# Performance work log

Measured on AMD Instinct MI355X. Metric: run time of the kernel, lower is better.

Reference implementation:

```python
import jax, jax.numpy as jnp
import numpy as np

B, C, H, W = 8, 192, 128, 128
NH, WS, PS = 6, 8, 8
HD = C // NH
SCALE = HD ** -0.5

def _rel_pos_log(ws):
    # log-spaced signed relative coordinates, [N, N, 2]
    coords = np.stack(np.meshgrid(np.arange(ws), np.arange(ws), indexing='ij'))
    cf = coords.reshape(2, -1)
    rp = (cf[:, :, None] - cf[:, None, :]).transpose(1, 2, 0).astype(np.float32)
    return jnp.asarray(np.sign(rp) * np.log1p(np.abs(rp)))

def setup_inputs() -> dict:
    key = jax.random.key(0)
    ks = jax.random.split(key, 8)
    s = 0.02
    return {
        'x': jax.random.normal(ks[0], (B, C, H, W), jnp.float32),
        'V_w': jax.random.normal(ks[1], (C, C), jnp.float32) * s,
        'V_b': jnp.zeros((C,), jnp.float32),
        'QK_w': jax.random.normal(ks[2], (2 * C, C), jnp.float32) * s,
        'QK_b': jnp.zeros((2 * C,), jnp.float32),
        'proj_w': jax.random.normal(ks[3], (C, C), jnp.float32) * s,
        'proj_b': jnp.zeros((C,), jnp.float32),
        'meta_w1': jax.random.normal(ks[4], (2, 256), jnp.float32) * s,
        'meta_b1': jnp.zeros((256,), jnp.float32),
        'meta_w2': jax.random.normal(ks[5], (256, NH), jnp.float32) * s,
        'meta_b2': jnp.zeros((NH,), jnp.float32),
    }

def reference(x, V_w, V_b, QK_w, QK_b, proj_w, proj_b, meta_w1, meta_b1, meta_w2, meta_b2):
    N = WS * WS
    # 1x1 convs for V and QK
    v = jnp.einsum('bchw,oc->bohw', x, V_w) + V_b[None, :, None, None]
    qk = jnp.einsum('bchw,oc->bohw', x, QK_w) + QK_b[None, :, None, None]
    qkv = jnp.concatenate([qk, v], axis=1)  # [B, 3C, H, W]
    # window partition -> [B * nW, N, 3C]
    t = qkv.transpose(0, 2, 3, 1).reshape(B, H // WS, WS, W // WS, WS, 3 * C)
    wins = t.transpose(0, 1, 3, 2, 4, 5).reshape(-1, N, 3 * C)
    B_ = wins.shape[0]
    qkv3 = wins.reshape(B_, N, 3, NH, HD).transpose(2, 0, 3, 1, 4)
    q, k, vv = qkv3[0] * SCALE, qkv3[1], qkv3[2]  # [B_, NH, N, HD]
    # FFT cross-modulation of q and k over the 8x8 window grid (c = N/64 = 1)
    cg = N // (PS * PS)
    qp = q.reshape(B_, NH, cg, PS, PS, HD).transpose(0, 1, 2, 5, 3, 4)
    kp = k.reshape(B_, NH, cg, PS, PS, HD).transpose(0, 1, 2, 5, 3, 4)
    o = jnp.fft.irfft2(jnp.fft.rfft2(qp) * jnp.fft.rfft2(kp), s=(PS, PS))
    o = o.transpose(0, 1, 2, 4, 5, 3).reshape(B_, NH, N, HD)
    # relative position bias from meta MLP on log-spaced coords
    rp = _rel_pos_log(WS)  # [N, N, 2]
    bias = jax.nn.relu(rp @ meta_w1 + meta_b1) @ meta_w2 + meta_b2  # [N, N, NH]
    bias = bias.transpose(2, 0, 1)  # [NH, N, N]
    attn = jnp.einsum('bhnd,bhmd->bhnm', o, vv) + bias[None]
    attn = jax.nn.softmax(attn, axis=-1)
    y = jnp.einsum('bhnm,bhmd->bhnd', attn, vv).transpose(0, 2, 1, 3).reshape(B_, N, C)
    # window reverse -> [B, C, H, W]
    y = y.reshape(B, H // WS, W // WS, WS, WS, C).transpose(0, 1, 3, 2, 4, 5).reshape(B, H, W, C)
    y = y.transpose(0, 3, 1, 2)
    return jnp.einsum('bchw,oc->bohw', y, proj_w) + proj_b[None, :, None, None]
```

## Files before the change

### kernel.cpp

```cpp
#include <hip/hip_runtime.h>

#define SCALEQ 0.17677669529663687f

typedef __bf16 bf16x8 __attribute__((ext_vector_type(8)));
typedef __bf16 bf16x2 __attribute__((ext_vector_type(2)));
typedef float f32x4 __attribute__((ext_vector_type(4)));
typedef float f32x2 __attribute__((ext_vector_type(2)));

__device__ __forceinline__ float bflo(unsigned int u) { return __uint_as_float(u << 16); }
__device__ __forceinline__ float bfhi(unsigned int u) { return __uint_as_float(u & 0xffff0000u); }
__device__ __forceinline__ f32x2 b2x2(unsigned int u) {
    f32x2 r; r[0] = bflo(u); r[1] = bfhi(u); return r;
}
__device__ __forceinline__ unsigned short f2b(float f) {
    return __builtin_bit_cast(unsigned short, (__bf16)f);
}
__device__ __forceinline__ unsigned int pk2(float a, float b) {
    bf16x2 v; v[0] = (__bf16)a; v[1] = (__bf16)b;
    return __builtin_bit_cast(unsigned int, v);
}

#define RA     0
#define RB     24576
#define RC     49152
#define LDS_BYTES 73728

#define WS_WQKV_ELEMS 110592
#define WS_WP_OFF_EL  110592
#define WS_B2_OFF_B   294912
#define WS_YB_OFF_B   393216
#define WS_TOTAL_B    50724864

__device__ __forceinline__ bf16x8 ldsf(const char* p) {
    uint4 u = *(const uint4*)p;
    return __builtin_bit_cast(bf16x8, u);
}
__device__ __forceinline__ bf16x8 gldf(const unsigned short* p) {
    uint4 u = *(const uint4*)p;
    return __builtin_bit_cast(bf16x8, u);
}

__global__ void wprep_kernel(const float* __restrict__ QKw, const float* __restrict__ Vw,
                             const float* __restrict__ Pw, unsigned short* __restrict__ wsb) {
    int i = blockIdx.x * 256 + threadIdx.x;
    if (i >= 147456) return;
    if (i < WS_WQKV_ELEMS) {
        int r = i / 192, c = i - r * 192;
        float v = (r < 384) ? QKw[r * 192 + c] : Vw[(r - 384) * 192 + c];
        if (r < 192) v *= SCALEQ;
        wsb[i] = f2b(v);
    } else {
        int j = i - WS_WQKV_ELEMS;
        wsb[WS_WP_OFF_EL + j] = f2b(Pw[j]);
    }
}

__global__ void bias2_kernel(const float* __restrict__ Mw1, const float* __restrict__ Mb1,
                             const float* __restrict__ Mw2, const float* __restrict__ Mb2,
                             float* __restrict__ out) {
    int i = blockIdx.x * 256 + threadIdx.x;
    if (i >= 6 * 64 * 64) return;
    int h = i >> 12, n = (i >> 6) & 63, m = i & 63;
    float dy = (float)((n >> 3) - (m >> 3));
    float dx = (float)((n & 7) - (m & 7));
    float f0 = copysignf(log1pf(fabsf(dy)), dy);
    float f1 = copysignf(log1pf(fabsf(dx)), dx);
    float a = Mb2[h];
    for (int u = 0; u < 256; ++u) {
        float hv = fmaxf(f0 * Mw1[u] + f1 * Mw1[256 + u] + Mb1[u], 0.0f);
        a = fmaf(hv, Mw2[u * 6 + h], a);
    }
    out[i] = a;
}

__global__ __launch_bounds__(512, 4)
void fused_win_attn(const float* __restrict__ x,
                    const float* __restrict__ Vb, const float* __restrict__ QKb,
                    const float* __restrict__ Pb,
                    const unsigned short* __restrict__ wqkv,
                    const unsigned short* __restrict__ wp,
                    const float* __restrict__ bias2,
                    char* __restrict__ yb,
                    float* __restrict__ out,
                    int split)
{
    extern __shared__ char smem[];
    const int t   = threadIdx.x;
    const int wv  = t >> 6;
    const int l15 = t & 15;
    const int l4  = (t >> 4) & 3;

    const int wid = ((blockIdx.x & 7) << 8) | (blockIdx.x >> 3);
    const int b   = wid >> 8;
    const int wy  = (wid >> 4) & 15;
    const int wx  = wid & 15;
    const int y0  = wy * 8, x0 = wx * 8;

    const f32x4 zz = {0.0f, 0.0f, 0.0f, 0.0f};

    {
        const float* xb = x + (size_t)b * 192 * 16384;
        #pragma unroll
        for (int i = 0; i < 6; ++i) {
            int idx = t + 512 * i;
            int c = idx >> 4, sub = idx & 15;
            int r = sub >> 1, hf = sub & 1;
            float4 v4 = *(const float4*)(xb + c * 16384 + (y0 + r) * 128 + x0 + hf * 4);
            int n0 = r * 8 + hf * 4;
            unsigned short sv[4] = {f2b(v4.x), f2b(v4.y), f2b(v4.z), f2b(v4.w)};
            #pragma unroll
            for (int e = 0; e < 4; ++e) {
                int n = n0 + e;
                *(unsigned short*)(smem + RA + ((n * 384 + c * 2) ^ ((n & 7) << 4))) = sv[e];
            }
        }
    }
    __syncthreads();

    const int wcol = wv & 3, wrow = wv >> 2;
    unsigned int vp[3][2][2];
    {
        bf16x8 afr[6][2];
        #pragma unroll
        for (int ks = 0; ks < 6; ++ks)
            #pragma unroll
            for (int mtl = 0; mtl < 2; ++mtl) {
                int row = (wrow * 2 + mtl) * 16 + l15;
                afr[ks][mtl] = ldsf(smem + RA + ((row * 384 + ks * 64 + l4 * 16) ^ ((row & 7) << 4)));
            }
        __syncthreads();

        auto gemm3 = [&](int obase, f32x4 acc[3][2]) {
            bf16x8 bw[3][6];
            #pragma unroll
            for (int j = 0; j < 3; ++j) {
                const unsigned short* wr = wqkv + (size_t)(obase + j * 16 + l15) * 192 + l4 * 8;
                #pragma unroll
                for (int ks = 0; ks < 6; ++ks) bw[j][ks] = gldf(wr + ks * 32);
            }
            #pragma unroll
            for (int j = 0; j < 3; ++j) { acc[j][0] = zz; acc[j][1] = zz; }
            #pragma unroll
            for (int ks = 0; ks < 6; ++ks)
                #pragma unroll
                for (int j = 0; j < 3; ++j)
                    #pragma unroll
                    for (int mtl = 0; mtl < 2; ++mtl)
                        acc[j][mtl] = __builtin_amdgcn_mfma_f32_16x16x32_bf16(afr[ks][mtl], bw[j][ks], acc[j][mtl], 0, 0, 0);
        };

        {
            f32x4 acc[3][2];
            gemm3(wcol * 48, acc);
            #pragma unroll
            for (int j = 0; j < 3; ++j) {
                int och = wcol * 48 + j * 16 + l15;
                float bv = QKb[och] * SCALEQ;
                #pragma unroll
                for (int mtl = 0; mtl < 2; ++mtl)
                    #pragma unroll
                    for (int rr = 0; rr < 4; ++rr) {
                        int tok = (wrow * 2 + mtl) * 16 + l4 * 4 + rr;
                        *(unsigned short*)(smem + RA + ((tok * 384 + och * 2) ^ ((tok & 7) << 4)))
                            = f2b(acc[j][mtl][rr] + bv);
                    }
            }
        }
        {
            f32x4 acc[3][2];
            gemm3(192 + wcol * 48, acc);
            #pragma unroll
            for (int j = 0; j < 3; ++j) {
                int ch = wcol * 48 + j * 16 + l15;
                float bv = QKb[192 + ch];
                #pragma unroll
                for (int mtl = 0; mtl < 2; ++mtl)
                    #pragma unroll
                    for (int rr = 0; rr < 4; ++rr) {
                        int tok = (wrow * 2 + mtl) * 16 + l4 * 4 + rr;
                        *(unsigned short*)(smem + RB + ((tok * 384 + ch * 2) ^ ((tok & 7) << 4)))
                            = f2b(acc[j][mtl][rr] + bv);
                    }
            }
        }
        {
            f32x4 acc[3][2];
            gemm3(384 + wcol * 48, acc);
            #pragma unroll
            for (int j = 0; j < 3; ++j) {
                int ch = wcol * 48 + j * 16 + l15;
                float bv = Vb[ch];
                #pragma unroll
                for (int mtl = 0; mtl < 2; ++mtl) {
                    vp[j][mtl][0] = pk2(acc[j][mtl][0] + bv, acc[j][mtl][1] + bv);
                    vp[j][mtl][1] = pk2(acc[j][mtl][2] + bv, acc[j][mtl][3] + bv);
                }
            }
        }
    }
    __syncthreads();

    if (t < 384) {
        const int rn = t / 48, cc = t % 48;
        const int c0b = cc * 8;
        f32x2 acc[8][2];
        #pragma unroll
        for (int cn = 0; cn < 8; ++cn) {
            acc[cn][0] = (f32x2){0.0f, 0.0f};
            acc[cn][1] = (f32x2){0.0f, 0.0f};
        }
        #pragma unroll
        for (int kh = 0; kh < 2; ++kh) {
            uint2 karr[32];
            #pragma unroll
            for (int m = 0; m < 32; ++m) {
                int row = kh * 32 + m;
                karr[m] = *(const uint2*)(smem + RB + ((row * 384 + c0b) ^ ((row & 7) << 4)));
            }
            #pragma unroll
            for (int mrl = 0; mrl < 4; ++mrl) {
                const int mr = kh * 4 + mrl;
                f32x2 kf[8][2];
                #pragma unroll
                for (int mc = 0; mc < 8; ++mc) {
                    uint2 kv = karr[mrl * 8 + mc];
                    kf[mc][0] = b2x2(kv.x); kf[mc][1] = b2x2(kv.y);
                }
                const int npr = (rn - mr) & 7;
                #pragma unroll
                for (int npc = 0; npc < 8; ++npc) {
                    int np = npr * 8 + npc;
                    uint2 qv = *(const uint2*)(smem + RA + ((np * 384 + c0b) ^ ((np & 7) << 4)));
                    f32x2 qf0 = b2x2(qv.x), qf1 = b2x2(qv.y);
                    #pragma unroll
                    for (int mc = 0; mc < 8; ++mc) {
                        int cn = (npc + mc) & 7;
                        acc[cn][0] = qf0 * kf[mc][0] + acc[cn][0];
                        acc[cn][1] = qf1 * kf[mc][1] + acc[cn][1];
                    }
                }
            }
        }
        #pragma unroll
        for (int cn = 0; cn < 8; ++cn) {
            int n = rn * 8 + cn;
            uint2 pk;
            pk.x = pk2(acc[cn][0][0], acc[cn][0][1]);
            pk.y = pk2(acc[cn][1][0], acc[cn][1][1]);
            *(uint2*)(smem + RC + ((n * 384 + c0b) ^ ((n & 7) << 4))) = pk;
        }
    }
    __syncthreads();

    {
        #pragma unroll
        for (int j = 0; j < 3; ++j) {
            int ch = wcol * 48 + j * 16 + l15;
            #pragma unroll
            for (int mtl = 0; mtl < 2; ++mtl)
                #pragma unroll
                for (int pp = 0; pp < 2; ++pp) {
                    unsigned int pk = vp[j][mtl][pp];
                    int tok0 = (wrow * 2 + mtl) * 16 + l4 * 4 + pp * 2;
                    *(unsigned int*)(smem + RB + ((ch * 128 + tok0 * 2) ^ ((ch & 7) << 4))) = pk;
                    *(unsigned short*)(smem + RA + ((tok0 * 384 + ch * 2) ^ ((tok0 & 7) << 4)))
                        = (unsigned short)(pk & 0xffffu);
                    *(unsigned short*)(smem + RA + (((tok0 + 1) * 384 + ch * 2) ^ (((tok0 + 1) & 7) << 4)))
                        = (unsigned short)(pk >> 16);
                }
        }
    }
    __syncthreads();

    unsigned int pv[3][4][2];
    {
        #pragma unroll
        for (int i = 0; i < 3; ++i) {
            int u = wv * 3 + i;
            int h = u >> 2, nt = u & 3;
            int brow = nt * 16 + l15;
            bf16x8 ofr = ldsf(smem + RC + ((brow * 384 + h * 64 + l4 * 16) ^ ((brow & 7) << 4)));
            int n = nt * 16 + l15;
            const float* bp = bias2 + ((h * 64 + n) << 6) + l4 * 4;
            float s[4][4];
            #pragma unroll
            for (int mt = 0; mt < 4; ++mt) {
                int arow = mt * 16 + l15;
                bf16x8 vfr = ldsf(smem + RA + ((arow * 384 + h * 64 + l4 * 16) ^ ((arow & 7) << 4)));
                f32x4 a = __builtin_amdgcn_mfma_f32_16x16x32_bf16(vfr, ofr, zz, 0, 0, 0);
                float4 bb = *(const float4*)(bp + mt * 16);
                s[mt][0] = a[0] + bb.x; s[mt][1] = a[1] + bb.y;
                s[mt][2] = a[2] + bb.z; s[mt][3] = a[3] + bb.w;
            }
            float m0 = s[0][0];
            #pragma unroll
            for (int mt = 0; mt < 4; ++mt)
                #pragma unroll
                for (int rr = 0; rr < 4; ++rr) m0 = fmaxf(m0, s[mt][rr]);
            m0 = fmaxf(m0, __shfl_xor(m0, 16));
            m0 = fmaxf(m0, __shfl_xor(m0, 32));
            float sm = 0.0f;
            #pragma unroll
            for (int mt = 0; mt < 4; ++mt)
                #pragma unroll
                for (int rr = 0; rr < 4; ++rr) {
                    float p = __expf(s[mt][rr] - m0);
                    s[mt][rr] = p; sm += p;
                }
            sm += __shfl_xor(sm, 16);
            sm += __shfl_xor(sm, 32);
            float inv = 1.0f / sm;
            #pragma unroll
            for (int mt = 0; mt < 4; ++mt) {
                pv[i][mt][0] = pk2(s[mt][0] * inv, s[mt][1] * inv);
                pv[i][mt][1] = pk2(s[mt][2] * inv, s[mt][3] * inv);
            }
        }
    }
    __syncthreads();

    {
        #pragma unroll
        for (int i = 0; i < 3; ++i) {
            int u = wv * 3 + i;
            int h = u >> 2, nt = u & 3;
            bf16x8 pafr[2];
            #pragma unroll
            for (int ks = 0; ks < 2; ++ks) {
                unsigned int au[4];
                #pragma unroll
                for (int p = 0; p < 4; ++p) {
                    int srcl4 = (2 * l4 + (p >> 1)) & 3;
                    int src = srcl4 * 16 + l15;
                    unsigned int v0 = (unsigned int)__shfl((int)pv[i][2 * ks][p & 1], src, 64);
                    unsigned int v1 = (unsigned int)__shfl((int)pv[i][2 * ks + 1][p & 1], src, 64);
                    au[p] = (l4 & 2) ? v1 : v0;
                }
                uint4 u4 = {au[0], au[1], au[2], au[3]};
                pafr[ks] = __builtin_bit_cast(bf16x8, u4);
            }
            f32x4 acc[2];
            acc[0] = zz; acc[1] = zz;
            #pragma unroll
            for (int dt = 0; dt < 2; ++dt)
                #pragma unroll
                for (int ks = 0; ks < 2; ++ks) {
                    int drow = h * 32 + dt * 16 + l15;
                    bf16x8 vtf = ldsf(smem + RB + ((drow * 128 + ks * 64 + l4 * 16) ^ ((drow & 7) << 4)));
                    acc[dt] = __builtin_amdgcn_mfma_f32_16x16x32_bf16(pafr[ks], vtf, acc[dt], 0, 0, 0);
                }
            #pragma unroll
            for (int dt = 0; dt < 2; ++dt)
                #pragma unroll
                for (int rr = 0; rr < 4; ++rr) {
                    int tok = nt * 16 + l4 * 4 + rr;
                    int ch  = h * 32 + dt * 16 + l15;
                    *(unsigned short*)(smem + RC + ((tok * 384 + ch * 2) ^ ((tok & 7) << 4))) = f2b(acc[dt][rr]);
                }
        }
    }
    __syncthreads();

    if (split) {
        char* ybw = yb + (size_t)wid * 24576;
        #pragma unroll
        for (int c = 0; c < 3; ++c) {
            int idx = t + 512 * c;
            uint4 v = *(const uint4*)(smem + RC + idx * 16);
            *(uint4*)(ybw + idx * 16) = v;
        }
        return;
    }

    {
        const int wc = wv & 3, wr = wv >> 2;
        bf16x8 wfr[3][6];
        #pragma unroll
        for (int jt = 0; jt < 3; ++jt) {
            int oc = wc * 48 + jt * 16;
            const unsigned short* wr_ = wp + (size_t)(oc + l15) * 192 + l4 * 8;
            #pragma unroll
            for (int ks = 0; ks < 6; ++ks) wfr[jt][ks] = gldf(wr_ + ks * 32);
        }
        f32x4 acc[3][2];
        #pragma unroll
        for (int jt = 0; jt < 3; ++jt) { acc[jt][0] = zz; acc[jt][1] = zz; }

        #pragma unroll
        for (int ks = 0; ks < 6; ++ks) {
            bf16x8 bfr[2];
            #pragma unroll
            for (int ntl = 0; ntl < 2; ++ntl) {
                int tok = (wr * 2 + ntl) * 16 + l15;
                bfr[ntl] = ldsf(smem + RC + ((tok * 384 + ks * 64 + l4 * 16) ^ ((tok & 7) << 4)));
            }
            #pragma unroll
            for (int jt = 0; jt < 3; ++jt)
                #pragma unroll
                for (int ntl = 0; ntl < 2; ++ntl)
                    acc[jt][ntl] = __builtin_amdgcn_mfma_f32_16x16x32_bf16(wfr[jt][ks], bfr[ntl], acc[jt][ntl], 0, 0, 0);
        }
        #pragma unroll
        for (int jt = 0; jt < 3; ++jt)
            #pragma unroll
            for (int rr = 0; rr < 4; ++rr) {
                int oc = wc * 48 + jt * 16 + l4 * 4 + rr;
                float pb = Pb[oc];
                float* obase = out + (size_t)(b * 192 + oc) * 16384;
                #pragma unroll
                for (int ntl = 0; ntl < 2; ++ntl) {
                    int tok = (wr * 2 + ntl) * 16 + l15;
                    obase[(y0 + (tok >> 3)) * 128 + x0 + (tok & 7)] = acc[jt][ntl][rr] + pb;
                }
            }
    }
}

__global__ __launch_bounds__(256)
void proj_kernel(const char* __restrict__ yb,
                 const unsigned short* __restrict__ wp,
                 const float* __restrict__ Pb,
                 float* __restrict__ out)
{
    extern __shared__ char smem[];
    const int t   = threadIdx.x;
    const int wv  = t >> 6;
    const int l15 = t & 15;
    const int l4  = (t >> 4) & 3;

    const int by = blockIdx.x;
    const int b  = by >> 7;
    const int y  = by & 127;
    const int wy = y >> 3, row = y & 7;

    const f32x4 zz = {0.0f, 0.0f, 0.0f, 0.0f};

    #pragma unroll
    for (int k = 0; k < 12; ++k) {
        int i = t + 256 * k;
        int px = i / 24, cb = i % 24;
        int wx = px >> 3, col = px & 7;
        const char* src = yb + (size_t)(((b * 16 + wy) * 16 + wx)) * 24576
                        + row * 3072 + col * 384 + cb * 16;
        uint4 v = *(const uint4*)src;
        *(uint4*)(smem + px * 384 + cb * 16) = v;
    }
    __syncthreads();

    bf16x8 wfr[3][6];
    #pragma unroll
    for (int jt = 0; jt < 3; ++jt) {
        int oc = wv * 48 + jt * 16;
        const unsigned short* wr_ = wp + (size_t)(oc + l15) * 192 + l4 * 8;
        #pragma unroll
        for (int ks = 0; ks < 6; ++ks) wfr[jt][ks] = gldf(wr_ + ks * 32);
    }
    #pragma unroll
    for (int half = 0; half < 2; ++half) {
        f32x4 acc[3][4];
        #pragma unroll
        for (int jt = 0; jt < 3; ++jt)
            #pragma unroll
            for (int ntl = 0; ntl < 4; ++ntl) acc[jt][ntl] = zz;
        #pragma unroll
        for (int ks = 0; ks < 6; ++ks) {
            bf16x8 bfr[4];
            #pragma unroll
            for (int ntl = 0; ntl < 4; ++ntl) {
                int px = (half * 4 + ntl) * 16 + l15;
                bfr[ntl] = ldsf(smem + ((px * 384 + ks * 64 + l4 * 16) ^ ((px & 7) << 4)));
            }
            #pragma unroll
            for (int jt = 0; jt < 3; ++jt)
                #pragma unroll
                for (int ntl = 0; ntl < 4; ++ntl)
                    acc[jt][ntl] = __builtin_amdgcn_mfma_f32_16x16x32_bf16(wfr[jt][ks], bfr[ntl], acc[jt][ntl], 0, 0, 0);
        }
        #pragma unroll
        for (int jt = 0; jt < 3; ++jt)
            #pragma unroll
            for (int rr = 0; rr < 4; ++rr) {
                int oc = wv * 48 + jt * 16 + l4 * 4 + rr;
                float pb = Pb[oc];
                float* op = out + ((size_t)(b * 192 + oc) * 128 + y) * 128;
                #pragma unroll
                for (int ntl = 0; ntl < 4; ++ntl) {
                    int px = (half * 4 + ntl) * 16 + l15;
                    op[px] = acc[jt][ntl][rr] + pb;
                }
            }
    }
}

extern "C" void kernel_launch(void* const* d_in, const int* in_sizes, int n_in,
                              void* d_out, int out_size, void* d_ws, size_t ws_size,
                              hipStream_t stream) {
    const float* x   = (const float*)d_in[0];
    const float* Vw  = (const float*)d_in[1];
    const float* Vb  = (const float*)d_in[2];
    const float* QKw = (const float*)d_in[3];
    const float* QKb = (const float*)d_in[4];
    const float* Pw  = (const float*)d_in[5];
    const float* Pb  = (const float*)d_in[6];
    const float* Mw1 = (const float*)d_in[7];
    const float* Mb1 = (const float*)d_in[8];
    const float* Mw2 = (const float*)d_in[9];
    const float* Mb2 = (const float*)d_in[10];
    float* outp = (float*)d_out;

    unsigned short* wsb = (unsigned short*)d_ws;
    float* b2 = (float*)((char*)d_ws + WS_B2_OFF_B);
    char* ybp = (char*)d_ws + WS_YB_OFF_B;
    const int split = (ws_size >= (size_t)WS_TOTAL_B) ? 1 : 0;

    wprep_kernel<<<dim3(576), dim3(256), 0, stream>>>(QKw, Vw, Pw, wsb);
    bias2_kernel<<<dim3(96), dim3(256), 0, stream>>>(Mw1, Mb1, Mw2, Mb2, b2);

    (void)hipFuncSetAttribute((const void*)fused_win_attn,
                              hipFuncAttributeMaxDynamicSharedMemorySize, LDS_BYTES);
    fused_win_attn<<<dim3(2048), dim3(512), LDS_BYTES, stream>>>(
        x, Vb, QKb, Pb, wsb, wsb + WS_WP_OFF_EL, b2, ybp, outp, split);

    if (split) {
        (void)hipFuncSetAttribute((const void*)proj_kernel,
                                  hipFuncAttributeMaxDynamicSharedMemorySize, 49152);
        proj_kernel<<<dim3(1024), dim3(256), 49152, stream>>>(
            ybp, wsb + WS_WP_OFF_EL, Pb, outp);
    }
}
```

Before: 292.0 us.

## Widen fused window attention block to 768 threads and redistribute work

Raises the fused window-attention block from 512 to 768 threads (12 waves) and remaps every phase onto the wider block. Each wave now covers two 48-channel chunks of the QKV GEMM, the FFT-modulation stage uses all 768 threads with 4-byte channel slices, attention runs two units per wave, and the projection gives each wave a 16-output-channel tile across all tokens. The aim is more parallelism and latency hiding per window. In exchange, the launch bound of 768 threads with 6 blocks caps registers per thread more tightly, which risks spills, and the V values are written to LDS by only half the waves.

```diff
diff --git a/kernel.cpp b/kernel.cpp
--- a/kernel.cpp
+++ b/kernel.cpp
@@ -73,7 +73,7 @@
     out[i] = a;
 }
 
-__global__ __launch_bounds__(512, 4)
+__global__ __launch_bounds__(768, 6)
 void fused_win_attn(const float* __restrict__ x,
                     const float* __restrict__ Vb, const float* __restrict__ QKb,
                     const float* __restrict__ Pb,
@@ -101,8 +101,8 @@
     {
         const float* xb = x + (size_t)b * 192 * 16384;
         #pragma unroll
-        for (int i = 0; i < 6; ++i) {
-            int idx = t + 512 * i;
+        for (int i = 0; i < 4; ++i) {
+            int idx = t + 768 * i;
             int c = idx >> 4, sub = idx & 15;
             int r = sub >> 1, hf = sub & 1;
             float4 v4 = *(const float4*)(xb + c * 16384 + (y0 + r) * 128 + x0 + hf * 4);
@@ -117,8 +117,8 @@
     }
     __syncthreads();
 
-    const int wcol = wv & 3, wrow = wv >> 2;
-    unsigned int vp[3][2][2];
+    const int wcol = wv >> 1, wrow = wv & 1;
+    unsigned int vp[2][3][2][2];
     {
         bf16x8 afr[6][2];
         #pragma unroll
@@ -130,7 +130,9 @@
             }
         __syncthreads();
 
-        auto gemm3 = [&](int obase, f32x4 acc[3][2]) {
+        #pragma unroll
+        for (int chunk = 0; chunk < 2; ++chunk) {
+            const int obase = wcol * 96 + chunk * 48;
             bf16x8 bw[3][6];
             #pragma unroll
             for (int j = 0; j < 3; ++j) {
@@ -138,6 +140,7 @@
                 #pragma unroll
                 for (int ks = 0; ks < 6; ++ks) bw[j][ks] = gldf(wr + ks * 32);
             }
+            f32x4 acc[3][2];
             #pragma unroll
             for (int j = 0; j < 3; ++j) { acc[j][0] = zz; acc[j][1] = zz; }
             #pragma unroll
@@ -147,96 +150,82 @@
                     #pragma unroll
                     for (int mtl = 0; mtl < 2; ++mtl)
                         acc[j][mtl] = __builtin_amdgcn_mfma_f32_16x16x32_bf16(afr[ks][mtl], bw[j][ks], acc[j][mtl], 0, 0, 0);
-        };
-
-        {
-            f32x4 acc[3][2];
-            gemm3(wcol * 48, acc);
-            #pragma unroll
-            for (int j = 0; j < 3; ++j) {
-                int och = wcol * 48 + j * 16 + l15;
-                float bv = QKb[och] * SCALEQ;
-                #pragma unroll
-                for (int mtl = 0; mtl < 2; ++mtl)
+
+            if (obase < 192) {
+                #pragma unroll
+                for (int j = 0; j < 3; ++j) {
+                    int och = obase + j * 16 + l15;
+                    float bv = QKb[och] * SCALEQ;
                     #pragma unroll
-                    for (int rr = 0; rr < 4; ++rr) {
-                        int tok = (wrow * 2 + mtl) * 16 + l4 * 4 + rr;
-                        *(unsigned short*)(smem + RA + ((tok * 384 + och * 2) ^ ((tok & 7) << 4)))
-                            = f2b(acc[j][mtl][rr] + bv);
+                    for (int mtl = 0; mtl < 2; ++mtl)
+                        #pragma unroll
+                        for (int rr = 0; rr < 4; ++rr) {
+                            int tok = (wrow * 2 + mtl) * 16 + l4 * 4 + rr;
+                            *(unsigned short*)(smem + RA + ((tok * 384 + och * 2) ^ ((tok & 7) << 4)))
+                                = f2b(acc[j][mtl][rr] + bv);
+                        }
+                }
+            } else if (obase < 384) {
+                #pragma unroll
+                for (int j = 0; j < 3; ++j) {
+                    int ch = obase - 192 + j * 16 + l15;
+                    float bv = QKb[192 + ch];
+                    #pragma unroll
+                    for (int mtl = 0; mtl < 2; ++mtl)
+                        #pragma unroll
+                        for (int rr = 0; rr < 4; ++rr) {
+                            int tok = (wrow * 2 + mtl) * 16 + l4 * 4 + rr;
+                            *(unsigned short*)(smem + RB + ((tok * 384 + ch * 2) ^ ((tok & 7) << 4)))
+                                = f2b(acc[j][mtl][rr] + bv);
+                        }
+                }
+            } else {
+                #pragma unroll
+                for (int j = 0; j < 3; ++j) {
+                    int ch = obase - 384 + j * 16 + l15;
+                    float bv = Vb[ch];
+                    #pragma unroll
+                    for (int mtl = 0; mtl < 2; ++mtl) {
+                        vp[chunk][j][mtl][0] = pk2(acc[j][mtl][0] + bv, acc[j][mtl][1] + bv);
+                        vp[chunk][j][mtl][1] = pk2(acc[j][mtl][2] + bv, acc[j][mtl][3] + bv);
                     }
-            }
-        }
-        {
-            f32x4 acc[3][2];
-            gemm3(192 + wcol * 48, acc);
-            #pragma unroll
-            for (int j = 0; j < 3; ++j) {
-                int ch = wcol * 48 + j * 16 + l15;
-                float bv = QKb[192 + ch];
-                #pragma unroll
-                for (int mtl = 0; mtl < 2; ++mtl)
-                    #pragma unroll
-                    for (int rr = 0; rr < 4; ++rr) {
-                        int tok = (wrow * 2 + mtl) * 16 + l4 * 4 + rr;
-                        *(unsigned short*)(smem + RB + ((tok * 384 + ch * 2) ^ ((tok & 7) << 4)))
-                            = f2b(acc[j][mtl][rr] + bv);
-                    }
-            }
-        }
-        {
-            f32x4 acc[3][2];
-            gemm3(384 + wcol * 48, acc);
-            #pragma unroll
-            for (int j = 0; j < 3; ++j) {
-                int ch = wcol * 48 + j * 16 + l15;
-                float bv = Vb[ch];
-                #pragma unroll
-                for (int mtl = 0; mtl < 2; ++mtl) {
-                    vp[j][mtl][0] = pk2(acc[j][mtl][0] + bv, acc[j][mtl][1] + bv);
-                    vp[j][mtl][1] = pk2(acc[j][mtl][2] + bv, acc[j][mtl][3] + bv);
-                }
-            }
-        }
-    }
-    __syncthreads();
-
-    if (t < 384) {
-        const int rn = t / 48, cc = t % 48;
-        const int c0b = cc * 8;
-        f32x2 acc[8][2];
-        #pragma unroll
-        for (int cn = 0; cn < 8; ++cn) {
-            acc[cn][0] = (f32x2){0.0f, 0.0f};
-            acc[cn][1] = (f32x2){0.0f, 0.0f};
-        }
+                }
+            }
+        }
+    }
+    __syncthreads();
+
+    {
+        const int rn = t / 96, cc = t % 96;
+        const int c0b = cc * 4;
+        f32x2 acc[8];
+        #pragma unroll
+        for (int cn = 0; cn < 8; ++cn) acc[cn] = (f32x2){0.0f, 0.0f};
+
         #pragma unroll
         for (int kh = 0; kh < 2; ++kh) {
-            uint2 karr[32];
+            unsigned int karr[32];
             #pragma unroll
             for (int m = 0; m < 32; ++m) {
                 int row = kh * 32 + m;
-                karr[m] = *(const uint2*)(smem + RB + ((row * 384 + c0b) ^ ((row & 7) << 4)));
+                karr[m] = *(const unsigned int*)(smem + RB + ((row * 384 + c0b) ^ ((row & 7) << 4)));
             }
             #pragma unroll
             for (int mrl = 0; mrl < 4; ++mrl) {
                 const int mr = kh * 4 + mrl;
-                f32x2 kf[8][2];
-                #pragma unroll
-                for (int mc = 0; mc < 8; ++mc) {
-                    uint2 kv = karr[mrl * 8 + mc];
-                    kf[mc][0] = b2x2(kv.x); kf[mc][1] = b2x2(kv.y);
-                }
+                f32x2 kf[8];
+                #pragma unroll
+                for (int mc = 0; mc < 8; ++mc) kf[mc] = b2x2(karr[mrl * 8 + mc]);
                 const int npr = (rn - mr) & 7;
                 #pragma unroll
                 for (int npc = 0; npc < 8; ++npc) {
                     int np = npr * 8 + npc;
-                    uint2 qv = *(const uint2*)(smem + RA + ((np * 384 + c0b) ^ ((np & 7) << 4)));
-                    f32x2 qf0 = b2x2(qv.x), qf1 = b2x2(qv.y);
+                    unsigned int qv = *(const unsigned int*)(smem + RA + ((np * 384 + c0b) ^ ((np & 7) << 4)));
+                    f32x2 qf = b2x2(qv);
                     #pragma unroll
                     for (int mc = 0; mc < 8; ++mc) {
                         int cn = (npc + mc) & 7;
-                        acc[cn][0] = qf0 * kf[mc][0] + acc[cn][0];
-                        acc[cn][1] = qf1 * kf[mc][1] + acc[cn][1];
+                        acc[cn] = qf * kf[mc] + acc[cn];
                     }
                 }
             }
@@ -244,39 +233,39 @@
         #pragma unroll
         for (int cn = 0; cn < 8; ++cn) {
             int n = rn * 8 + cn;
-            uint2 pk;
-            pk.x = pk2(acc[cn][0][0], acc[cn][0][1]);
-            pk.y = pk2(acc[cn][1][0], acc[cn][1][1]);
-            *(uint2*)(smem + RC + ((n * 384 + c0b) ^ ((n & 7) << 4))) = pk;
-        }
-    }
-    __syncthreads();
-
+            unsigned int pk = pk2(acc[cn][0], acc[cn][1]);
+            *(unsigned int*)(smem + RC + ((n * 384 + c0b) ^ ((n & 7) << 4))) = pk;
+        }
+    }
+    __syncthreads();
+
+    if (wcol >= 4) {
+        #pragma unroll
+        for (int chunk = 0; chunk < 2; ++chunk)
+            #pragma unroll
+            for (int j = 0; j < 3; ++j) {
+                int ch = (wcol - 4) * 96 + chunk * 48 + j * 16 + l15;
+                #pragma unroll
+                for (int mtl = 0; mtl < 2; ++mtl)
+                    #pragma unroll
+                    for (int pp = 0; pp < 2; ++pp) {
+                        unsigned int pk = vp[chunk][j][mtl][pp];
+                        int tok0 = (wrow * 2 + mtl) * 16 + l4 * 4 + pp * 2;
+                        *(unsigned int*)(smem + RB + ((ch * 128 + tok0 * 2) ^ ((ch & 7) << 4))) = pk;
+                        *(unsigned short*)(smem + RA + ((tok0 * 384 + ch * 2) ^ ((tok0 & 7) << 4)))
+                            = (unsigned short)(pk & 0xffffu);
+                        *(unsigned short*)(smem + RA + (((tok0 + 1) * 384 + ch * 2) ^ (((tok0 + 1) & 7) << 4)))
+                            = (unsigned short)(pk >> 16);
+                    }
+            }
+    }
+    __syncthreads();
+
+    unsigned int pv[2][4][2];
     {
         #pragma unroll
-        for (int j = 0; j < 3; ++j) {
-            int ch = wcol * 48 + j * 16 + l15;
-            #pragma unroll
-            for (int mtl = 0; mtl < 2; ++mtl)
-                #pragma unroll
-                for (int pp = 0; pp < 2; ++pp) {
-                    unsigned int pk = vp[j][mtl][pp];
-                    int tok0 = (wrow * 2 + mtl) * 16 + l4 * 4 + pp * 2;
-                    *(unsigned int*)(smem + RB + ((ch * 128 + tok0 * 2) ^ ((ch & 7) << 4))) = pk;
-                    *(unsigned short*)(smem + RA + ((tok0 * 384 + ch * 2) ^ ((tok0 & 7) << 4)))
-                        = (unsigned short)(pk & 0xffffu);
-                    *(unsigned short*)(smem + RA + (((tok0 + 1) * 384 + ch * 2) ^ (((tok0 + 1) & 7) << 4)))
-                        = (unsigned short)(pk >> 16);
-                }
-        }
-    }
-    __syncthreads();
-
-    unsigned int pv[3][4][2];
-    {
-        #pragma unroll
-        for (int i = 0; i < 3; ++i) {
-            int u = wv * 3 + i;
+        for (int i = 0; i < 2; ++i) {
+            int u = wv * 2 + i;
             int h = u >> 2, nt = u & 3;
             int brow = nt * 16 + l15;
             bf16x8 ofr = ldsf(smem + RC + ((brow * 384 + h * 64 + l4 * 16) ^ ((brow & 7) << 4)));
@@ -321,8 +310,8 @@
 
     {
         #pragma unroll
-        for (int i = 0; i < 3; ++i) {
-            int u = wv * 3 + i;
+        for (int i = 0; i < 2; ++i) {
+            int u = wv * 2 + i;
             int h = u >> 2, nt = u & 3;
             bf16x8 pafr[2];
             #pragma unroll
@@ -364,8 +353,8 @@
     if (split) {
         char* ybw = yb + (size_t)wid * 24576;
         #pragma unroll
-        for (int c = 0; c < 3; ++c) {
-            int idx = t + 512 * c;
+        for (int c = 0; c < 2; ++c) {
+            int idx = t + 768 * c;
             uint4 v = *(const uint4*)(smem + RC + idx * 16);
             *(uint4*)(ybw + idx * 16) = v;
         }
@@ -373,46 +362,32 @@
     }
 
     {
-        const int wc = wv & 3, wr = wv >> 2;
-        bf16x8 wfr[3][6];
-        #pragma unroll
-        for (int jt = 0; jt < 3; ++jt) {
-            int oc = wc * 48 + jt * 16;
-            const unsigned short* wr_ = wp + (size_t)(oc + l15) * 192 + l4 * 8;
-            #pragma unroll
-            for (int ks = 0; ks < 6; ++ks) wfr[jt][ks] = gldf(wr_ + ks * 32);
-        }
-        f32x4 acc[3][2];
-        #pragma unroll
-        for (int jt = 0; jt < 3; ++jt) { acc[jt][0] = zz; acc[jt][1] = zz; }
-
-        #pragma unroll
-        for (int ks = 0; ks < 6; ++ks) {
-            bf16x8 bfr[2];
-            #pragma unroll
-            for (int ntl = 0; ntl < 2; ++ntl) {
-                int tok = (wr * 2 + ntl) * 16 + l15;
-                bfr[ntl] = ldsf(smem + RC + ((tok * 384 + ks * 64 + l4 * 16) ^ ((tok & 7) << 4)));
-            }
-            #pragma unroll
-            for (int jt = 0; jt < 3; ++jt)
-                #pragma unroll
-                for (int ntl = 0; ntl < 2; ++ntl)
-                    acc[jt][ntl] = __builtin_amdgcn_mfma_f32_16x16x32_bf16(wfr[jt][ks], bfr[ntl], acc[jt][ntl], 0, 0, 0);
-        }
-        #pragma unroll
-        for (int jt = 0; jt < 3; ++jt)
-            #pragma unroll
-            for (int rr = 0; rr < 4; ++rr) {
-                int oc = wc * 48 + jt * 16 + l4 * 4 + rr;
-                float pb = Pb[oc];
-                float* obase = out + (size_t)(b * 192 + oc) * 16384;
-                #pragma unroll
-                for (int ntl = 0; ntl < 2; ++ntl) {
-                    int tok = (wr * 2 + ntl) * 16 + l15;
-                    obase[(y0 + (tok >> 3)) * 128 + x0 + (tok & 7)] = acc[jt][ntl][rr] + pb;
-                }
-            }
+        bf16x8 wfr[6];
+        const unsigned short* wr_ = wp + (size_t)(wv * 16 + l15) * 192 + l4 * 8;
+        #pragma unroll
+        for (int ks = 0; ks < 6; ++ks) wfr[ks] = gldf(wr_ + ks * 32);
+        f32x4 acc[4];
+        #pragma unroll
+        for (int ntl = 0; ntl < 4; ++ntl) acc[ntl] = zz;
+        #pragma unroll
+        for (int ks = 0; ks < 6; ++ks)
+            #pragma unroll
+            for (int ntl = 0; ntl < 4; ++ntl) {
+                int tok = ntl * 16 + l15;
+                bf16x8 bfr = ldsf(smem + RC + ((tok * 384 + ks * 64 + l4 * 16) ^ ((tok & 7) << 4)));
+                acc[ntl] = __builtin_amdgcn_mfma_f32_16x16x32_bf16(wfr[ks], bfr, acc[ntl], 0, 0, 0);
+            }
+        #pragma unroll
+        for (int rr = 0; rr < 4; ++rr) {
+            int oc = wv * 16 + l4 * 4 + rr;
+            float pb = Pb[oc];
+            float* obase = out + (size_t)(b * 192 + oc) * 16384;
+            #pragma unroll
+            for (int ntl = 0; ntl < 4; ++ntl) {
+                int tok = ntl * 16 + l15;
+                obase[(y0 + (tok >> 3)) * 128 + x0 + (tok & 7)] = acc[ntl][rr] + pb;
+            }
+        }
     }
 }
 
@@ -518,7 +493,7 @@
 
     (void)hipFuncSetAttribute((const void*)fused_win_attn,
                               hipFuncAttributeMaxDynamicSharedMemorySize, LDS_BYTES);
-    fused_win_attn<<<dim3(2048), dim3(512), LDS_BYTES, stream>>>(
+    fused_win_attn<<<dim3(2048), dim3(768), LDS_BYTES, stream>>>(
         x, Vb, QKb, Pb, wsb, wsb + WS_WP_OFF_EL, b2, ybp, outp, split);
 
     if (split) {
```

Result: slower. 355.8 us (+21.8%).

## Pre-pack input windows into bf16 swizzled slabs in a separate kernel

Applied to the files above, without the earlier changes.

Adds an xprep kernel that converts x to bf16 and writes each 8x8 window as a pre-swizzled contiguous slab in workspace. The fused attention kernel then loads its input with contiguous 16-byte copies instead of strided fp32 gathers and scattered 2-byte LDS stores. The y output reuses the same slab buffer in place. It also merges the weight-prep and bias kernels into one launch. The cost is an extra pass over x through global memory plus one more launch.

```diff
diff --git a/kernel.cpp b/kernel.cpp
--- a/kernel.cpp
+++ b/kernel.cpp
@@ -28,7 +28,7 @@
 #define WS_WQKV_ELEMS 110592
 #define WS_WP_OFF_EL  110592
 #define WS_B2_OFF_B   294912
-#define WS_YB_OFF_B   393216
+#define WS_SLAB_OFF_B 393216
 #define WS_TOTAL_B    50724864
 
 __device__ __forceinline__ bf16x8 ldsf(const char* p) {
@@ -40,37 +40,58 @@
     return __builtin_bit_cast(bf16x8, u);
 }
 
-__global__ void wprep_kernel(const float* __restrict__ QKw, const float* __restrict__ Vw,
-                             const float* __restrict__ Pw, unsigned short* __restrict__ wsb) {
-    int i = blockIdx.x * 256 + threadIdx.x;
-    if (i >= 147456) return;
-    if (i < WS_WQKV_ELEMS) {
-        int r = i / 192, c = i - r * 192;
+__global__ void prep_kernel(const float* __restrict__ QKw, const float* __restrict__ Vw,
+                            const float* __restrict__ Pw,
+                            const float* __restrict__ Mw1, const float* __restrict__ Mb1,
+                            const float* __restrict__ Mw2, const float* __restrict__ Mb2,
+                            unsigned short* __restrict__ wsb, float* __restrict__ b2) {
+    int gid = blockIdx.x * 256 + threadIdx.x;
+    if (gid < WS_WQKV_ELEMS) {
+        int r = gid / 192, c = gid - r * 192;
         float v = (r < 384) ? QKw[r * 192 + c] : Vw[(r - 384) * 192 + c];
         if (r < 192) v *= SCALEQ;
-        wsb[i] = f2b(v);
+        wsb[gid] = f2b(v);
+    } else if (gid < 147456) {
+        int j = gid - WS_WQKV_ELEMS;
+        wsb[WS_WP_OFF_EL + j] = f2b(Pw[j]);
     } else {
-        int j = i - WS_WQKV_ELEMS;
-        wsb[WS_WP_OFF_EL + j] = f2b(Pw[j]);
-    }
-}
-
-__global__ void bias2_kernel(const float* __restrict__ Mw1, const float* __restrict__ Mb1,
-                             const float* __restrict__ Mw2, const float* __restrict__ Mb2,
-                             float* __restrict__ out) {
-    int i = blockIdx.x * 256 + threadIdx.x;
-    if (i >= 6 * 64 * 64) return;
-    int h = i >> 12, n = (i >> 6) & 63, m = i & 63;
-    float dy = (float)((n >> 3) - (m >> 3));
-    float dx = (float)((n & 7) - (m & 7));
-    float f0 = copysignf(log1pf(fabsf(dy)), dy);
-    float f1 = copysignf(log1pf(fabsf(dx)), dx);
-    float a = Mb2[h];
-    for (int u = 0; u < 256; ++u) {
-        float hv = fmaxf(f0 * Mw1[u] + f1 * Mw1[256 + u] + Mb1[u], 0.0f);
-        a = fmaf(hv, Mw2[u * 6 + h], a);
-    }
-    out[i] = a;
+        int i = gid - 147456;
+        int h = i >> 12, n = (i >> 6) & 63, m = i & 63;
+        float dy = (float)((n >> 3) - (m >> 3));
+        float dx = (float)((n & 7) - (m & 7));
+        float f0 = copysignf(log1pf(fabsf(dy)), dy);
+        float f1 = copysignf(log1pf(fabsf(dx)), dx);
+        float a = Mb2[h];
+        for (int u = 0; u < 256; ++u) {
+            float hv = fmaxf(f0 * Mw1[u] + f1 * Mw1[256 + u] + Mb1[u], 0.0f);
+            a = fmaf(hv, Mw2[u * 6 + h], a);
+        }
+        b2[i] = a;
+    }
+}
+
+__global__ __launch_bounds__(256)
+void xprep_kernel(const float* __restrict__ x, char* __restrict__ xw) {
+    int blk = blockIdx.x;
+    int b = blk >> 6, wy = (blk >> 2) & 15, wxg = blk & 3;
+    const float* xb = x + (size_t)b * 192 * 16384;
+    #pragma unroll 4
+    for (int i = 0; i < 48; ++i) {
+        int idx = threadIdx.x + 256 * i;
+        int c = idx >> 6, rem = idx & 63;
+        int r = rem >> 3, g = rem & 7;
+        float4 v4 = *(const float4*)(xb + c * 16384 + (wy * 8 + r) * 128 + wxg * 32 + g * 4);
+        int wx  = wxg * 4 + (g >> 1);
+        int wid = (b << 8) | (wy << 4) | wx;
+        char* slab = xw + (size_t)wid * 24576;
+        int n0 = r * 8 + (g & 1) * 4;
+        unsigned short sv[4] = {f2b(v4.x), f2b(v4.y), f2b(v4.z), f2b(v4.w)};
+        #pragma unroll
+        for (int e = 0; e < 4; ++e) {
+            int n = n0 + e;
+            *(unsigned short*)(slab + ((n * 384 + c * 2) ^ ((n & 7) << 4))) = sv[e];
+        }
+    }
 }
 
 __global__ __launch_bounds__(512, 4)
@@ -80,7 +101,7 @@
                     const unsigned short* __restrict__ wqkv,
                     const unsigned short* __restrict__ wp,
                     const float* __restrict__ bias2,
-                    char* __restrict__ yb,
+                    char* __restrict__ slabs,
                     float* __restrict__ out,
                     int split)
 {
@@ -98,7 +119,15 @@
 
     const f32x4 zz = {0.0f, 0.0f, 0.0f, 0.0f};
 
-    {
+    if (split) {
+        const char* slab = slabs + (size_t)wid * 24576;
+        #pragma unroll
+        for (int i = 0; i < 3; ++i) {
+            int idx = t + 512 * i;
+            uint4 v = *(const uint4*)(slab + idx * 16);
+            *(uint4*)(smem + RA + idx * 16) = v;
+        }
+    } else {
         const float* xb = x + (size_t)b * 192 * 16384;
         #pragma unroll
         for (int i = 0; i < 6; ++i) {
@@ -362,7 +391,7 @@
     __syncthreads();
 
     if (split) {
-        char* ybw = yb + (size_t)wid * 24576;
+        char* ybw = slabs + (size_t)wid * 24576;
         #pragma unroll
         for (int c = 0; c < 3; ++c) {
             int idx = t + 512 * c;
@@ -510,21 +539,22 @@
 
     unsigned short* wsb = (unsigned short*)d_ws;
     float* b2 = (float*)((char*)d_ws + WS_B2_OFF_B);
-    char* ybp = (char*)d_ws + WS_YB_OFF_B;
+    char* slabs = (char*)d_ws + WS_SLAB_OFF_B;
     const int split = (ws_size >= (size_t)WS_TOTAL_B) ? 1 : 0;
 
-    wprep_kernel<<<dim3(576), dim3(256), 0, stream>>>(QKw, Vw, Pw, wsb);
-    bias2_kernel<<<dim3(96), dim3(256), 0, stream>>>(Mw1, Mb1, Mw2, Mb2, b2);
+    prep_kernel<<<dim3(672), dim3(256), 0, stream>>>(QKw, Vw, Pw, Mw1, Mb1, Mw2, Mb2, wsb, b2);
+    if (split)
+        xprep_kernel<<<dim3(512), dim3(256), 0, stream>>>(x, slabs);
 
     (void)hipFuncSetAttribute((const void*)fused_win_attn,
                               hipFuncAttributeMaxDynamicSharedMemorySize, LDS_BYTES);
     fused_win_attn<<<dim3(2048), dim3(512), LDS_BYTES, stream>>>(
-        x, Vb, QKb, Pb, wsb, wsb + WS_WP_OFF_EL, b2, ybp, outp, split);
+        x, Vb, QKb, Pb, wsb, wsb + WS_WP_OFF_EL, b2, slabs, outp, split);
 
     if (split) {
         (void)hipFuncSetAttribute((const void*)proj_kernel,
                                   hipFuncAttributeMaxDynamicSharedMemorySize, 49152);
         proj_kernel<<<dim3(1024), dim3(256), 49152, stream>>>(
-            ybp, wsb + WS_WP_OFF_EL, Pb, outp);
-    }
-}
+            slabs, wsb + WS_WP_OFF_EL, Pb, outp);
+    }
+}
```

After: 382.6 us. 31.0% more time.
